# Performance work log

Measured on AMD Instinct MI355X. Metric: run time of the kernel, lower is better.

The kernel has to match this reference:

```python
import jax, jax.numpy as jnp
import numpy as np

N, L, D = 1024, 128, 512
H = D // 2  # LSTM hidden per direction


def _lstm_dir(x, w_ih, w_hh, b_ih, b_hh, reverse=False):
    # x: [B, T, Din] -> [B, T, H]; PyTorch gate order i, f, g, o
    B = x.shape[0]
    Hh = w_hh.shape[1]
    xs = jnp.swapaxes(x, 0, 1)  # [T, B, Din]
    if reverse:
        xs = xs[::-1]
    pre = jnp.einsum('tbi,gi->tbg', xs, w_ih) + b_ih  # precompute input contribution

    def step(carry, p):
        h, c = carry
        g = p + h @ w_hh.T + b_hh
        i, f, cc, o = jnp.split(g, 4, axis=-1)
        c = jax.nn.sigmoid(f) * c + jax.nn.sigmoid(i) * jnp.tanh(cc)
        h = jax.nn.sigmoid(o) * jnp.tanh(c)
        return (h, c), h

    zeros = jnp.zeros((B, Hh), x.dtype)
    _, hs = jax.lax.scan(step, (zeros, zeros), pre)
    if reverse:
        hs = hs[::-1]
    return jnp.swapaxes(hs, 0, 1)


def _bilstm(x, params):
    # params: [(w_ih, w_hh, b_ih, b_hh)] for l0_fwd, l0_bwd, l1_fwd, l1_bwd
    for lf, lb in ((params[0], params[1]), (params[2], params[3])):
        f = _lstm_dir(x, *lf)
        b = _lstm_dir(x, *lb, reverse=True)
        x = jnp.concatenate([f, b], axis=-1)
    return x


def _forward(episodes, query, current_state, ages, Wq, bq, Wk, bk, lstm_params, k):
    # retrieve_relevant_episodes: batched version of the per-episode loop
    query_proj = query @ Wq.T + bq              # [D]
    emb = episodes.mean(axis=1)                 # [N, D] per-episode mean embedding
    key_proj = emb @ Wk.T + bk                  # [N, D]
    scores = key_proj @ query_proj              # [N] (matmul(q, kp.T).mean() == dot for 1D)
    _, idx = jax.lax.top_k(scores, k)           # descending, == argsort[-k:][::-1]
    sel = jnp.take(episodes, idx, axis=0)       # [k, L, D]
    # temporal_attention
    w = 1.0 / (1.0 + jnp.take(ages, idx) * 0.01)  # temporal recency weight
    x = sel * w[:, None, None]
    lstm_out = _bilstm(x, lstm_params)          # [k, L, D]
    att = jnp.einsum('d,kld->kl', current_state, lstm_out)  # [k, L] (== [k,1,L])
    attw = jax.nn.softmax(att, axis=-1)
    context = jnp.einsum('kl,kld->kd', attw, lstm_out)[:, None, :]  # [k, 1, D]
    return context


def setup_inputs() -> dict:
    key = jax.random.key(0)
    ks = jax.random.split(key, 32)
    s = 1.0 / np.sqrt(D)
    sh = 1.0 / np.sqrt(H)
    inp = {
        'episodes': jax.random.normal(ks[0], (N, L, D), jnp.float32),
        'query': jax.random.normal(ks[1], (D,), jnp.float32),
        'current_state': jax.random.normal(ks[2], (D,), jnp.float32),
        'ages': jax.random.uniform(ks[3], (N,), jnp.float32) * 100.0,
        'Wq': jax.random.normal(ks[4], (D, D), jnp.float32) * s,
        'bq': jnp.zeros((D,), jnp.float32),
        'Wk': jax.random.normal(ks[5], (D, D), jnp.float32) * s,
        'bk': jnp.zeros((D,), jnp.float32),
    }
    i = 6
    for name in ['l0', 'l0r', 'l1', 'l1r']:
        inp['w_ih_' + name] = jax.random.normal(ks[i], (4 * H, D), jnp.float32) * sh; i += 1
        inp['w_hh_' + name] = jax.random.normal(ks[i], (4 * H, H), jnp.float32) * sh; i += 1
        inp['b_ih_' + name] = jnp.zeros((4 * H,), jnp.float32)
        inp['b_hh_' + name] = jnp.zeros((4 * H,), jnp.float32)
    inp['k'] = 5
    return inp


def reference(episodes, query, current_state, ages, Wq, bq, Wk, bk,
              w_ih_l0, w_hh_l0, b_ih_l0, b_hh_l0,
              w_ih_l0r, w_hh_l0r, b_ih_l0r, b_hh_l0r,
              w_ih_l1, w_hh_l1, b_ih_l1, b_hh_l1,
              w_ih_l1r, w_hh_l1r, b_ih_l1r, b_hh_l1r, k):
    lstm_params = [
        (w_ih_l0, w_hh_l0, b_ih_l0, b_hh_l0),
        (w_ih_l0r, w_hh_l0r, b_ih_l0r, b_hh_l0r),
        (w_ih_l1, w_hh_l1, b_ih_l1, b_hh_l1),
        (w_ih_l1r, w_hh_l1r, b_ih_l1r, b_hh_l1r),
    ]
    return _forward(episodes, query, current_state, ages, Wq, bq, Wk, bk, lstm_params, k)
```

## Files before the change

### kernel.cpp

```cpp
#include <hip/hip_runtime.h>
#include <hip/hip_bf16.h>
#include <math.h>

typedef unsigned short u16;
typedef unsigned int   u32;
typedef unsigned long long u64;

#define DEV static __device__ __forceinline__

static constexpr int LL = 128, DD = 512, HH = 256, KK = 5, NN = 1024;

static constexpr size_t OFF_QP   = 0;
static constexpr size_t OFF_U    = 4096;
static constexpr size_t OFF_CC   = 8192;
static constexpr size_t OFF_SC   = 12288;
static constexpr size_t OFF_WSC  = 16384;
static constexpr size_t OFF_IDX  = 16640;
static constexpr size_t OFF_HG   = 20480;
static constexpr size_t OFF_FLG0 = 61440;
static constexpr size_t OFF_FLG1 = 65536;
static constexpr size_t OFF_PRE  = 73728;
static constexpr size_t OFF_OUT0 = OFF_PRE  + (size_t)2*LL*5*1024*4;
static constexpr size_t OFF_OUT1 = OFF_OUT0 + (size_t)5*LL*DD*4;

DEV float sigf(float x){ return 1.0f/(1.0f + expf(-x)); }

__global__ void k_qproj(const float* __restrict__ Wq, const float* __restrict__ q,
                        const float* __restrict__ bq, float* __restrict__ qp) {
  __shared__ float qs[512];
  int tid = threadIdx.x;
  qs[tid] = q[tid]; qs[tid+256] = q[tid+256];
  __syncthreads();
  int row  = blockIdx.x*8 + (tid >> 5);
  int lane = tid & 31;
  const float* wr = Wq + (size_t)row*512 + lane*16;
  float acc = 0.f;
  #pragma unroll
  for (int j = 0; j < 16; j += 4) {
    float4 w = *(const float4*)(wr + j);
    acc += w.x*qs[lane*16+j] + w.y*qs[lane*16+j+1] + w.z*qs[lane*16+j+2] + w.w*qs[lane*16+j+3];
  }
  #pragma unroll
  for (int off = 16; off > 0; off >>= 1) acc += __shfl_down(acc, off, 32);
  if (lane == 0) qp[row] = acc + bq[row];
}

__global__ void k_keyvec(const float* __restrict__ Wk, const float* __restrict__ bk,
                         const float* __restrict__ qp, float* __restrict__ u,
                         float* __restrict__ cconst) {
  __shared__ float qs[512];
  __shared__ float red[16][17];
  __shared__ float r2[256];
  int tid = threadIdx.x;
  qs[tid] = qp[tid]; qs[tid+256] = qp[tid+256];
  __syncthreads();
  int cl = tid & 15;
  int jc = tid >> 4;
  int col = blockIdx.x*16 + cl;
  float acc = 0.f;
  for (int j = jc*32; j < jc*32 + 32; ++j) acc += Wk[(size_t)j*512 + col] * qs[j];
  red[cl][jc] = acc;
  __syncthreads();
  if (tid < 16) {
    float a = 0.f;
    #pragma unroll
    for (int m = 0; m < 16; ++m) a += red[tid][m];
    u[blockIdx.x*16 + tid] = a;
  }
  if (blockIdx.x == 0) {
    float b2 = bk[tid]*qs[tid] + bk[tid+256]*qs[tid+256];
    r2[tid] = b2;
    __syncthreads();
    for (int off = 128; off > 0; off >>= 1) { if (tid < off) r2[tid] += r2[tid+off]; __syncthreads(); }
    if (tid == 0) cconst[0] = r2[0];
  }
}

__global__ void k_scores(const float* __restrict__ ep, const float* __restrict__ u,
                         const float* __restrict__ cconst, float* __restrict__ scores) {
  __shared__ float red[256];
  int tid = threadIdx.x, n = blockIdx.x;
  int d0 = (tid * 4) & 511;
  float u0 = u[d0+0], u1 = u[d0+1], u2 = u[d0+2], u3 = u[d0+3];
  const float* base = ep + (size_t)n * (LL*DD);
  float acc = 0.f;
  for (int c = tid; c < (LL*DD)/4; c += 256) {
    float4 v = *(const float4*)(base + (size_t)c*4);
    acc += v.x*u0 + v.y*u1 + v.z*u2 + v.w*u3;
  }
  red[tid] = acc;
  __syncthreads();
  for (int off = 128; off > 0; off >>= 1) { if (tid < off) red[tid] += red[tid+off]; __syncthreads(); }
  if (tid == 0) scores[n] = red[0] * (1.0f/LL) + cconst[0];
}

__global__ void k_topk(const float* __restrict__ scores, const float* __restrict__ ages,
                       int* __restrict__ idx5, float* __restrict__ wsc) {
  __shared__ float s0[NN];
  __shared__ float sv[NN];
  __shared__ int   si[NN];
  __shared__ int   chosen[KK];
  int tid = threadIdx.x;
  s0[tid] = scores[tid];
  __syncthreads();
  for (int r = 0; r < KK; ++r) {
    float v = s0[tid];
    for (int m = 0; m < r; ++m) if (chosen[m] == tid) v = -3.4e38f;
    sv[tid] = v; si[tid] = tid;
    __syncthreads();
    for (int off = 512; off > 0; off >>= 1) {
      if (tid < off) {
        float a = sv[tid], b = sv[tid+off];
        int ia = si[tid], ib = si[tid+off];
        if (b > a || (b == a && ib < ia)) { sv[tid] = b; si[tid] = ib; }
      }
      __syncthreads();
    }
    if (tid == 0) {
      int w = si[0];
      chosen[r] = w;
      idx5[r] = w;
      wsc[r] = 1.0f / (1.0f + ages[w] * 0.01f);
    }
    __syncthreads();
  }
}

__global__ __launch_bounds__(256) void k_pre(
    const float* __restrict__ ep, const float* __restrict__ x1,
    const int* __restrict__ idx5, const float* __restrict__ wsc,
    const float* __restrict__ wihF, const float* __restrict__ wihB,
    const float* __restrict__ bihF, const float* __restrict__ bhhF,
    const float* __restrict__ bihB, const float* __restrict__ bhhB,
    float* __restrict__ pre) {
  int t = blockIdx.x, dir = blockIdx.y;
  int tid = threadIdx.x;
  __shared__ __align__(16) float xs[5*512];
  if (ep) {
    for (int f = tid; f < 5*512; f += 256) {
      int b = f >> 9, i = f & 511;
      xs[f] = ep[((size_t)idx5[b]*LL + t)*DD + i] * wsc[b];
    }
  } else {
    for (int f = tid; f < 5*512; f += 256) {
      int b = f >> 9, i = f & 511;
      xs[f] = x1[((size_t)b*LL + t)*DD + i];
    }
  }
  const float* wih = dir ? wihB : wihF;
  const float* bih = dir ? bihB : bihF;
  const float* bhh = dir ? bhhB : bhhF;
  __syncthreads();

  const float4* w4 = (const float4*)wih;
  const float4* x4 = (const float4*)xs;
  float acc[4][5];
  #pragma unroll
  for (int g = 0; g < 4; ++g)
    #pragma unroll
    for (int b = 0; b < 5; ++b) acc[g][b] = 0.f;

  #pragma unroll 4
  for (int kq = 0; kq < 128; ++kq) {
    float4 xv[5];
    #pragma unroll
    for (int b = 0; b < 5; ++b) xv[b] = x4[b*128 + kq];
    #pragma unroll
    for (int g = 0; g < 4; ++g) {
      float4 w = w4[(size_t)(tid + g*256)*128 + kq];
      #pragma unroll
      for (int b = 0; b < 5; ++b) {
        acc[g][b] += w.x*xv[b].x + w.y*xv[b].y + w.z*xv[b].z + w.w*xv[b].w;
      }
    }
  }

  size_t pbase = (((size_t)dir*LL + t)*5)*1024;
  #pragma unroll
  for (int g = 0; g < 4; ++g) {
    int row = tid + g*256;
    float bias = bih[row] + bhh[row];
    #pragma unroll
    for (int b = 0; b < 5; ++b)
      pre[pbase + (size_t)b*1024 + row] = acc[g][b] + bias;
  }
}

__global__ __launch_bounds__(1024) void k_lstm(
    const float* __restrict__ whhF, const float* __restrict__ whhB,
    const float* __restrict__ pre, float* __restrict__ out,
    float* __restrict__ hg, int* __restrict__ flg) {
  int wg  = blockIdx.x;
  int dir = wg >> 3;
  int q   = wg & 7;
  int tid = threadIdx.x;
  int p   = tid & 127;
  int jq  = tid >> 7;
  int jb  = jq * 32;
  const float* whh = dir ? whhB : whhF;

  __shared__ __align__(16) float h_lds[5*256];
  __shared__ float part[128*5*9];
  __shared__ float c_s[5*32];
  __shared__ float pre_lds[5*128];

  int gr = (p >> 5) * 256 + q * 32 + (p & 31);
  float w[32];
  #pragma unroll
  for (int m4 = 0; m4 < 8; ++m4) {
    float4 a = *(const float4*)(whh + (size_t)gr*256 + jb + m4*4);
    w[m4*4+0] = a.x; w[m4*4+1] = a.y; w[m4*4+2] = a.z; w[m4*4+3] = a.w;
  }
  for (int f = tid; f < 1280; f += 1024) h_lds[f] = 0.f;
  if (tid < 160) c_s[tid] = 0.f;
  float* hg_dir = hg + (size_t)dir * 2 * 1280;
  int*  flg_dir = flg + dir * 64;
  __syncthreads();

  for (int s = 0; s < LL; ++s) {
    int t = dir ? (LL-1-s) : s;
    if (tid < 640) {
      int b = tid >> 7, r = tid & 127;
      int grow = (r >> 5)*256 + q*32 + (r & 31);
      pre_lds[tid] = pre[(((size_t)dir*LL + t)*5 + b)*1024 + grow];
    }
    if (s > 0) {
      const float* hrd = hg_dir + (size_t)(s & 1) * 1280;
      if (tid < 8) {
        while (__hip_atomic_load(&flg_dir[tid], __ATOMIC_RELAXED,
                                 __HIP_MEMORY_SCOPE_AGENT) < s) {}
      }
      __syncthreads();
      for (int f = tid; f < 1120; f += 1024) {
        int b = f / 224, w2 = f % 224;
        int c7 = w2 >> 5, u = w2 & 31;
        int pch = c7 + (c7 >= q);
        int idx = b*256 + pch*32 + u;
        h_lds[idx] = __hip_atomic_load(&hrd[idx], __ATOMIC_RELAXED,
                                       __HIP_MEMORY_SCOPE_AGENT);
      }
    }
    __syncthreads();
    float acc[5];
    #pragma unroll
    for (int b = 0; b < 5; ++b) {
      const float4* h4 = (const float4*)&h_lds[b*256 + jb];
      float a = 0.f;
      #pragma unroll
      for (int m4 = 0; m4 < 8; ++m4) {
        float4 hv = h4[m4];
        a += w[m4*4+0]*hv.x + w[m4*4+1]*hv.y + w[m4*4+2]*hv.z + w[m4*4+3]*hv.w;
      }
      acc[b] = a;
    }
    #pragma unroll
    for (int b = 0; b < 5; ++b) part[(p*5 + b)*9 + jq] = acc[b];
    __syncthreads();
    if (tid < 160) {
      int b = tid >> 5, u = tid & 31;
      float g[4];
      #pragma unroll
      for (int gate = 0; gate < 4; ++gate) {
        int r = gate*32 + u;
        float sum = pre_lds[b*128 + r];
        #pragma unroll
        for (int m = 0; m < 8; ++m) sum += part[(r*5 + b)*9 + m];
        g[gate] = sum;
      }
      float ig = sigf(g[0]), fg = sigf(g[1]), cc = tanhf(g[2]), og = sigf(g[3]);
      float cn = fg * c_s[b*32 + u] + ig * cc;
      c_s[b*32 + u] = cn;
      float hv = og * tanhf(cn);
      out[((size_t)b*LL + t)*DD + dir*HH + q*32 + u] = hv;
      h_lds[b*256 + q*32 + u] = hv;
      float* hwr = hg_dir + (size_t)((s + 1) & 1) * 1280;
      __hip_atomic_store(&hwr[b*256 + q*32 + u], hv,
                         __ATOMIC_RELAXED, __HIP_MEMORY_SCOPE_AGENT);
    }
    __syncthreads();
    if (tid == 0)
      __hip_atomic_store(&flg_dir[q], s + 1, __ATOMIC_RELAXED,
                         __HIP_MEMORY_SCOPE_AGENT);
  }
}

__global__ void k_attn(const float* __restrict__ out1, const float* __restrict__ csb,
                       float* __restrict__ outp) {
  int b = blockIdx.x, tid = threadIdx.x;
  __shared__ float cs[512];
  __shared__ float att[128];
  __shared__ float red[256];
  __shared__ float smax, ssum;
  cs[tid] = csb[tid]; cs[tid+256] = csb[tid+256];
  __syncthreads();
  {
    int t = tid & 127, half = tid >> 7;
    const float* row = out1 + ((size_t)b*LL + t)*DD + half*256;
    const float* c2 = cs + half*256;
    float a = 0.f;
    for (int d = 0; d < 256; ++d) a += row[d] * c2[d];
    red[tid] = a;
  }
  __syncthreads();
  if (tid < 128) att[tid] = red[tid] + red[tid+128];
  __syncthreads();
  if (tid < 64) red[tid] = fmaxf(att[tid], att[tid+64]);
  __syncthreads();
  if (tid == 0) { float m = red[0]; for (int o = 1; o < 64; ++o) m = fmaxf(m, red[o]); smax = m; }
  __syncthreads();
  if (tid < 128) att[tid] = expf(att[tid] - smax);
  __syncthreads();
  if (tid < 64) red[tid] = att[tid] + att[tid+64];
  __syncthreads();
  if (tid == 0) { float s = 0.f; for (int o = 0; o < 64; ++o) s += red[o]; ssum = s; }
  __syncthreads();
  float inv = 1.0f / ssum;
  for (int d = tid; d < DD; d += 256) {
    float acc = 0.f;
    for (int t2 = 0; t2 < LL; ++t2) acc += att[t2] * out1[((size_t)b*LL + t2)*DD + d];
    outp[b*DD + d] = acc * inv;
  }
}

extern "C" void kernel_launch(void* const* d_in, const int* in_sizes, int n_in,
                              void* d_out, int out_size, void* d_ws, size_t ws_size,
                              hipStream_t stream) {
  (void)in_sizes; (void)n_in; (void)out_size; (void)ws_size;
  const float* ep   = (const float*)d_in[0];
  const float* qu   = (const float*)d_in[1];
  const float* cst  = (const float*)d_in[2];
  const float* ages = (const float*)d_in[3];
  const float* Wq   = (const float*)d_in[4];
  const float* bq   = (const float*)d_in[5];
  const float* Wk   = (const float*)d_in[6];
  const float* bk   = (const float*)d_in[7];
  const float *wih[4], *whh[4], *bih[4], *bhh[4];
  for (int l = 0; l < 4; ++l) {
    wih[l] = (const float*)d_in[8 + l*4 + 0];
    whh[l] = (const float*)d_in[8 + l*4 + 1];
    bih[l] = (const float*)d_in[8 + l*4 + 2];
    bhh[l] = (const float*)d_in[8 + l*4 + 3];
  }
  char* ws = (char*)d_ws;
  float* qp   = (float*)(ws + OFF_QP);
  float* uvec = (float*)(ws + OFF_U);
  float* cc   = (float*)(ws + OFF_CC);
  float* sc   = (float*)(ws + OFF_SC);
  float* wsc  = (float*)(ws + OFF_WSC);
  int*   idx5 = (int*)  (ws + OFF_IDX);
  float* hg0  = (float*)(ws + OFF_HG);
  float* hg1  = (float*)(ws + OFF_HG + 20480);
  int*   flg0 = (int*)  (ws + OFF_FLG0);
  int*   flg1 = (int*)  (ws + OFF_FLG1);
  float* pre  = (float*)(ws + OFF_PRE);
  float* out0 = (float*)(ws + OFF_OUT0);
  float* out1 = (float*)(ws + OFF_OUT1);

  hipMemsetAsync(ws + OFF_FLG0, 0, 8192, stream);

  k_qproj <<<64, 256, 0, stream>>>(Wq, qu, bq, qp);
  k_keyvec<<<32, 256, 0, stream>>>(Wk, bk, qp, uvec, cc);
  k_scores<<<NN, 256, 0, stream>>>(ep, uvec, cc, sc);
  k_topk  <<<1, 1024, 0, stream>>>(sc, ages, idx5, wsc);

  k_pre <<<dim3(LL,2), 256, 0, stream>>>(ep, nullptr, idx5, wsc,
        wih[0], wih[1], bih[0], bhh[0], bih[1], bhh[1], pre);
  k_lstm<<<16, 1024, 0, stream>>>(whh[0], whh[1], pre, out0, hg0, flg0);

  k_pre <<<dim3(LL,2), 256, 0, stream>>>(nullptr, out0, idx5, wsc,
        wih[2], wih[3], bih[2], bhh[2], bih[3], bhh[3], pre);
  k_lstm<<<16, 1024, 0, stream>>>(whh[2], whh[3], pre, out1, hg1, flg1);

  k_attn<<<KK, 256, 0, stream>>>(out1, cst, (float*)d_out);
}
```

Baseline: 1.451 ms.

## Repartition LSTM recurrent matvec to two rows per thread with 16-wide K slices

Each thread now computes two gate rows over a 16-element slice of the hidden state instead of one row over a 32-element slice, so every h vector loaded from LDS is reused across two weight rows. The partial-sum buffer is re-laid out so each thread writes a float2, and the gate reduction now sums 16 partials per row instead of 8. This halves LDS reads of h per FMA but doubles the serial reduction work done by the 160 gate threads on every timestep.

```diff
diff --git a/kernel.cpp b/kernel.cpp
--- a/kernel.cpp
+++ b/kernel.cpp
@@ -194,22 +194,26 @@
   int dir = wg >> 3;
   int q   = wg & 7;
   int tid = threadIdx.x;
-  int p   = tid & 127;
-  int jq  = tid >> 7;
-  int jb  = jq * 32;
+  int rp  = tid & 63;
+  int jq  = tid >> 6;
+  int jb  = jq * 16;
   const float* whh = dir ? whhB : whhF;
 
   __shared__ __align__(16) float h_lds[5*256];
-  __shared__ float part[128*5*9];
+  __shared__ __align__(16) float part[5*16*130];
   __shared__ float c_s[5*32];
   __shared__ float pre_lds[5*128];
 
-  int gr = (p >> 5) * 256 + q * 32 + (p & 31);
-  float w[32];
-  #pragma unroll
-  for (int m4 = 0; m4 < 8; ++m4) {
-    float4 a = *(const float4*)(whh + (size_t)gr*256 + jb + m4*4);
-    w[m4*4+0] = a.x; w[m4*4+1] = a.y; w[m4*4+2] = a.z; w[m4*4+3] = a.w;
+  int r0 = 2*rp, r1 = 2*rp + 1;
+  int gr0 = (r0 >> 5)*256 + q*32 + (r0 & 31);
+  int gr1 = (r1 >> 5)*256 + q*32 + (r1 & 31);
+  float w0[16], w1[16];
+  #pragma unroll
+  for (int m4 = 0; m4 < 4; ++m4) {
+    float4 a = *(const float4*)(whh + (size_t)gr0*256 + jb + m4*4);
+    w0[m4*4+0]=a.x; w0[m4*4+1]=a.y; w0[m4*4+2]=a.z; w0[m4*4+3]=a.w;
+    float4 c = *(const float4*)(whh + (size_t)gr1*256 + jb + m4*4);
+    w1[m4*4+0]=c.x; w1[m4*4+1]=c.y; w1[m4*4+2]=c.z; w1[m4*4+3]=c.w;
   }
   for (int f = tid; f < 1280; f += 1024) h_lds[f] = 0.f;
   if (tid < 160) c_s[tid] = 0.f;
@@ -241,20 +245,25 @@
       }
     }
     __syncthreads();
-    float acc[5];
-    #pragma unroll
-    for (int b = 0; b < 5; ++b) {
-      const float4* h4 = (const float4*)&h_lds[b*256 + jb];
-      float a = 0.f;
+    {
+      float acc0[5], acc1[5];
       #pragma unroll
-      for (int m4 = 0; m4 < 8; ++m4) {
-        float4 hv = h4[m4];
-        a += w[m4*4+0]*hv.x + w[m4*4+1]*hv.y + w[m4*4+2]*hv.z + w[m4*4+3]*hv.w;
-      }
-      acc[b] = a;
-    }
-    #pragma unroll
-    for (int b = 0; b < 5; ++b) part[(p*5 + b)*9 + jq] = acc[b];
+      for (int b = 0; b < 5; ++b) {
+        const float4* h4 = (const float4*)&h_lds[b*256 + jb];
+        float a0 = 0.f, a1 = 0.f;
+        #pragma unroll
+        for (int m4 = 0; m4 < 4; ++m4) {
+          float4 hv = h4[m4];
+          a0 += w0[m4*4+0]*hv.x + w0[m4*4+1]*hv.y + w0[m4*4+2]*hv.z + w0[m4*4+3]*hv.w;
+          a1 += w1[m4*4+0]*hv.x + w1[m4*4+1]*hv.y + w1[m4*4+2]*hv.z + w1[m4*4+3]*hv.w;
+        }
+        acc0[b] = a0; acc1[b] = a1;
+      }
+      #pragma unroll
+      for (int b = 0; b < 5; ++b) {
+        *(float2*)&part[(b*16 + jq)*130 + 2*rp] = make_float2(acc0[b], acc1[b]);
+      }
+    }
     __syncthreads();
     if (tid < 160) {
       int b = tid >> 5, u = tid & 31;
@@ -264,7 +273,7 @@
         int r = gate*32 + u;
         float sum = pre_lds[b*128 + r];
         #pragma unroll
-        for (int m = 0; m < 8; ++m) sum += part[(r*5 + b)*9 + m];
+        for (int m = 0; m < 16; ++m) sum += part[(b*16 + m)*130 + r];
         g[gate] = sum;
       }
       float ig = sigf(g[0]), fg = sigf(g[1]), cc = tanhf(g[2]), og = sigf(g[3]);
```

Result: no change. 1.435 ms (-1.1%).
